# Kernel optimization log

Hardware: AMD Instinct MI355X
Metric: run time of the kernel (lower is better)

Reference implementation:

```python
import jax, jax.numpy as jnp
import numpy as np

B, N, IN_F, OUT_F, H = 16, 1024, 256, 256, 4
D = OUT_F // H  # head_dim = 64
NEG_SLOPE = 0.2


def setup_inputs() -> dict:
    key = jax.random.key(0)
    k1, k2, k3 = jax.random.split(key, 3)
    h = jax.random.normal(k1, (B, N, IN_F), dtype=jnp.float32)
    mask = jnp.ones((B, N), dtype=jnp.int32)
    W = jax.random.normal(k2, (OUT_F, IN_F), dtype=jnp.float32) * (1.0 / np.sqrt(IN_F))
    a = jax.random.normal(k3, (2 * D, 1), dtype=jnp.float32) * 0.1
    return {"h": h, "mask": mask, "W": W, "a": a}


def reference(h, mask, W, a):
    # Wh = h @ W.T -> (B, N, OUT_F) -> (B, H, N, D)
    Wh = jnp.einsum('bnf,of->bno', h, W)
    Wh = Wh.reshape(h.shape[0], h.shape[1], H, D).transpose(0, 2, 1, 3)
    # Additive split: cat([Wh_i, Wh_j]) @ a == Wh_i @ a1 + Wh_j @ a2 (same math,
    # avoids the O(N^2 * 2D) concat tensor)
    a1 = a[:D, 0]  # (D,)
    a2 = a[D:, 0]  # (D,)
    s1 = jnp.einsum('bhnd,d->bhn', Wh, a1)  # score for node i
    s2 = jnp.einsum('bhnd,d->bhn', Wh, a2)  # score for node j
    e = s1[:, :, :, None] + s2[:, :, None, :]          # (B, H, N, N)
    e = jnp.where(e >= 0, e, NEG_SLOPE * e)            # LeakyReLU(0.2)
    node_mask = mask.astype(bool)                      # (B, N)
    mm = node_mask[:, None, :, None] & node_mask[:, None, None, :]  # (B,1,N,N)
    e = jnp.where(mm, e, -jnp.inf)
    attn = jax.nn.softmax(e, axis=-1)
    # dropout is identity in eval mode
    attn = jnp.where(mm, attn, 0.0)
    h_prime = jnp.einsum('bhij,bhjd->bhid', attn, Wh)  # (B, H, N, D)
    h_prime = h_prime.transpose(0, 2, 1, 3).reshape(h.shape[0], h.shape[1], OUT_F)
    return h_prime * mask.astype(h_prime.dtype)[:, :, None]
```

## Files before the change

kernel.cpp:

```cpp
#include <hip/hip_runtime.h>

typedef short short8 __attribute__((ext_vector_type(8)));
typedef float floatx4 __attribute__((ext_vector_type(4)));
typedef float floatx16 __attribute__((ext_vector_type(16)));
typedef unsigned int u32;

#define NEG_SLOPE 0.2f

__device__ __forceinline__ u32 pk_rtne(float a, float b) {
    u32 ua = __float_as_uint(a); ua += 0x7fffu + ((ua >> 16) & 1u);
    u32 ub = __float_as_uint(b); ub += 0x7fffu + ((ub >> 16) & 1u);
    return __builtin_amdgcn_perm(ub, ua, 0x07060302);
}
__device__ __forceinline__ u32 pk_trunc(float a, float b) {
    return __builtin_amdgcn_perm(__float_as_uint(b), __float_as_uint(a), 0x07060302);
}
__device__ __forceinline__ void gl_lds16(const void* g, void* l) {
    __builtin_amdgcn_global_load_lds((__attribute__((address_space(1))) u32*)(void*)g,
                                     (__attribute__((address_space(3))) u32*)l, 16, 0, 0);
}

__global__ __launch_bounds__(256, 4) void k_wh(
    const float* __restrict__ hin, const int* __restrict__ mask,
    const float* __restrict__ W, const float* __restrict__ a,
    unsigned short* __restrict__ WhF, float2* __restrict__ E1F1,
    float2* __restrict__ E2F2)
{
    __shared__ unsigned short sBF[8 * 4 * 64 * 8];
    __shared__ float sV1[256], sV2[256];

    const int t = threadIdx.x;
    const int bi = blockIdx.x;
    const int mtile = bi & 255, hh = bi >> 8;
    const int m0g = mtile * 64;
    const int b = m0g >> 10, i0 = m0g & 1023;
    const int b4h = b * 4 + hh;
    const int wid = t >> 6, lane = t & 63;
    const int l15 = lane & 15, q = lane >> 4;

    sV1[t] = 0.f;
    sV2[t] = 0.f;
    __syncthreads();

    float vp1[8] = {0, 0, 0, 0, 0, 0, 0, 0};
    float vp2[8] = {0, 0, 0, 0, 0, 0, 0, 0};
    {
        const int c = t & 31;
        const int rb = t >> 5;
#pragma unroll
        for (int i = 0; i < 8; ++i) {
            int row = i * 8 + rb;
            const float* gp = &W[((size_t)(hh * 64 + row)) * 256 + c * 8];
            float4 w0 = *(const float4*)gp;
            float4 w1 = *(const float4*)(gp + 4);
            float a1r = a[row], a2r = a[64 + row];
            vp1[0] += a1r * w0.x; vp1[1] += a1r * w0.y; vp1[2] += a1r * w0.z; vp1[3] += a1r * w0.w;
            vp1[4] += a1r * w1.x; vp1[5] += a1r * w1.y; vp1[6] += a1r * w1.z; vp1[7] += a1r * w1.w;
            vp2[0] += a2r * w0.x; vp2[1] += a2r * w0.y; vp2[2] += a2r * w0.z; vp2[3] += a2r * w0.w;
            vp2[4] += a2r * w1.x; vp2[5] += a2r * w1.y; vp2[6] += a2r * w1.z; vp2[7] += a2r * w1.w;
            uint4 pv;
            pv.x = pk_rtne(w0.x, w0.y); pv.y = pk_rtne(w0.z, w0.w);
            pv.z = pk_rtne(w1.x, w1.y); pv.w = pk_rtne(w1.z, w1.w);
            int kt = c >> 2, qq = c & 3, nt = row >> 4, r15 = row & 15;
            int idx16 = (kt * 4 + nt) * 64 + qq * 16 + r15;
            *(uint4*)&sBF[(idx16 ^ kt) * 8] = pv;
        }
    }
#pragma unroll
    for (int j = 0; j < 8; ++j) {
        vp1[j] += __shfl_xor(vp1[j], 32, 64);
        vp2[j] += __shfl_xor(vp2[j], 32, 64);
    }
    if (lane < 32) {
        const int c = t & 31;
#pragma unroll
        for (int j = 0; j < 8; ++j) {
            atomicAdd(&sV1[c * 8 + j], vp1[j]);
            atomicAdd(&sV2[c * 8 + j], vp2[j]);
        }
    }
    __syncthreads();

    floatx4 acc[4];
#pragma unroll
    for (int nt = 0; nt < 4; ++nt) {
        floatx4 z = {0.f, 0.f, 0.f, 0.f};
        acc[nt] = z;
    }
    float s1a = 0.f, s2a = 0.f;
    const float* hrow = &hin[((size_t)(m0g + wid * 16 + l15)) * 256 + q * 8];
#pragma unroll
    for (int kt = 0; kt < 8; ++kt) {
        float4 h0 = *(const float4*)(hrow + kt * 32);
        float4 h1 = *(const float4*)(hrow + kt * 32 + 4);
        float4 v1a = *(const float4*)&sV1[kt * 32 + q * 8];
        float4 v1b = *(const float4*)&sV1[kt * 32 + q * 8 + 4];
        float4 v2a = *(const float4*)&sV2[kt * 32 + q * 8];
        float4 v2b = *(const float4*)&sV2[kt * 32 + q * 8 + 4];
        s1a += h0.x * v1a.x + h0.y * v1a.y + h0.z * v1a.z + h0.w * v1a.w
             + h1.x * v1b.x + h1.y * v1b.y + h1.z * v1b.z + h1.w * v1b.w;
        s2a += h0.x * v2a.x + h0.y * v2a.y + h0.z * v2a.z + h0.w * v2a.w
             + h1.x * v2b.x + h1.y * v2b.y + h1.z * v2b.z + h1.w * v2b.w;
        union { short8 s; uint4 u; } af;
        af.u.x = pk_rtne(h0.x, h0.y); af.u.y = pk_rtne(h0.z, h0.w);
        af.u.z = pk_rtne(h1.x, h1.y); af.u.w = pk_rtne(h1.z, h1.w);
#pragma unroll
        for (int nt = 0; nt < 4; ++nt) {
            int idx16 = (kt * 4 + nt) * 64 + lane;
            short8 bf = *(const short8*)&sBF[(idx16 ^ kt) * 8];
            acc[nt] = __builtin_amdgcn_mfma_f32_16x16x32_bf16(af.s, bf, acc[nt], 0, 0, 0);
        }
    }

    const int jt16 = (i0 >> 4) + wid;
    const int g = q & 1, jb = (q >> 1) * 4;
#pragma unroll
    for (int nt = 0; nt < 4; ++nt) {
        int nt32 = nt >> 1;
        int l31 = (nt & 1) * 16 + l15;
        uint2 pv;
        pv.x = pk_rtne(acc[nt][0], acc[nt][1]);
        pv.y = pk_rtne(acc[nt][2], acc[nt][3]);
        size_t idx = ((((size_t)b4h * 64 + jt16) * 2 + nt32) * 64 + (g * 32 + l31)) * 8 + jb;
        *(uint2*)&WhF[idx] = pv;
    }

    s1a += __shfl_xor(s1a, 16, 64); s1a += __shfl_xor(s1a, 32, 64);
    s2a += __shfl_xor(s2a, 16, 64); s2a += __shfl_xor(s2a, 32, 64);
    if (lane < 16) {
        int i = i0 + wid * 16 + lane;
        E1F1[(size_t)b4h * 1024 + i] = make_float2(__expf(s1a), __expf(NEG_SLOPE * s1a));
        int mj = mask[b * 1024 + i];
        E2F2[(size_t)b4h * 1024 + i] =
            make_float2(mj ? __expf(s2a) : 0.f, mj ? __expf(NEG_SLOPE * s2a) : 0.f);
    }
}

__global__ __launch_bounds__(256, 2) void k_attn(
    const int* __restrict__ mask,
    const unsigned short* __restrict__ WhF,
    const float2* __restrict__ E1F1, const float2* __restrict__ E2F2,
    float* __restrict__ out)
{
    __shared__ float2 sEF[1024];

    const int t = threadIdx.x;
    const int bi = blockIdx.x;
    const int b4h = bi & 63, ib = bi >> 6;
    const int b = b4h >> 2, hh = b4h & 3;
    const int i0 = ib * 128;
    const int wid = t >> 6, lane = t & 63;
    const int l31 = lane & 31, g = lane >> 5;
    const int iw = i0 + wid * 32;

    {
        const char* src = (const char*)(E2F2 + (size_t)b4h * 1024);
        gl_lds16(src + t * 16, (char*)sEF + t * 16);
        gl_lds16(src + 4096 + t * 16, (char*)sEF + 4096 + t * 16);
    }

    float2 e1 = E1F1[(size_t)b4h * 1024 + iw + l31];
    const float E1 = e1.x, F1 = e1.y;

    floatx16 acc0, acc1, accL;
#pragma unroll
    for (int r = 0; r < 16; ++r) { acc0[r] = 0.f; acc1[r] = 0.f; accL[r] = 0.f; }
    const short ob = (short)0x3F80;
    const short8 ones = {ob, ob, ob, ob, ob, ob, ob, ob};

    const char* gbase = (const char*)WhF + (size_t)b4h * 131072 + (size_t)lane * 16;

    __syncthreads();

    short8 nb0 = *(const short8*)(gbase);
    short8 nb1 = *(const short8*)(gbase + 1024);
    float4 nA0, nA1, nB0, nB1;
    {
        const float4* pA = (const float4*)&sEF[g * 4];
        const float4* pB = (const float4*)&sEF[8 + g * 4];
        nA0 = pA[0]; nA1 = pA[1]; nB0 = pB[0]; nB1 = pB[1];
    }

#pragma unroll 8
    for (int c = 0; c < 64; ++c) {
        const short8 bf0 = nb0, bf1 = nb1;
        const float4 eA0 = nA0, eA1 = nA1, eB0 = nB0, eB1 = nB1;
        {
            const int cn = (c + 1) & 63;
            nb0 = *(const short8*)(gbase + (size_t)cn * 2048);
            nb1 = *(const short8*)(gbase + (size_t)cn * 2048 + 1024);
            const float4* pA = (const float4*)&sEF[cn * 16 + g * 4];
            const float4* pB = (const float4*)&sEF[cn * 16 + 8 + g * 4];
            nA0 = pA[0]; nA1 = pA[1]; nB0 = pB[0]; nB1 = pB[1];
        }
        float w0 = fmaxf(E1 * eA0.x, F1 * eA0.y);
        float w1 = fmaxf(E1 * eA0.z, F1 * eA0.w);
        float w2 = fmaxf(E1 * eA1.x, F1 * eA1.y);
        float w3 = fmaxf(E1 * eA1.z, F1 * eA1.w);
        float w4 = fmaxf(E1 * eB0.x, F1 * eB0.y);
        float w5 = fmaxf(E1 * eB0.z, F1 * eB0.w);
        float w6 = fmaxf(E1 * eB1.x, F1 * eB1.y);
        float w7 = fmaxf(E1 * eB1.z, F1 * eB1.w);
        union { short8 s; u32 u[4]; } af;
        af.u[0] = pk_trunc(w0, w1);
        af.u[1] = pk_trunc(w2, w3);
        af.u[2] = pk_trunc(w4, w5);
        af.u[3] = pk_trunc(w6, w7);
        acc0 = __builtin_amdgcn_mfma_f32_32x32x16_bf16(af.s, bf0, acc0, 0, 0, 0);
        acc1 = __builtin_amdgcn_mfma_f32_32x32x16_bf16(af.s, bf1, acc1, 0, 0, 0);
        accL = __builtin_amdgcn_mfma_f32_32x32x16_bf16(af.s, ones, accL, 0, 0, 0);
    }

#pragma unroll
    for (int r = 0; r < 16; ++r) {
        int row = (r & 3) + 8 * (r >> 2) + 4 * g;
        int i = iw + row;
        float l = accL[r];
        int mi = mask[b * 1024 + i];
        float inv = (mi && l > 0.f) ? 1.0f / l : 0.f;
        size_t o = ((size_t)(b * 1024 + i)) * 256 + hh * 64;
        out[o + l31] = acc0[r] * inv;
        out[o + 32 + l31] = acc1[r] * inv;
    }
}

extern "C" void kernel_launch(void* const* d_in, const int* in_sizes, int n_in,
                              void* d_out, int out_size, void* d_ws, size_t ws_size,
                              hipStream_t stream) {
    const float* h = (const float*)d_in[0];
    const int* mask = (const int*)d_in[1];
    const float* W = (const float*)d_in[2];
    const float* a = (const float*)d_in[3];
    float* out = (float*)d_out;

    unsigned short* WhF = (unsigned short*)d_ws;
    float2* E1F1 = (float2*)((char*)d_ws + (size_t)64 * 64 * 2 * 64 * 8 * 2);
    float2* E2F2 = E1F1 + 64 * 1024;

    hipLaunchKernelGGL(k_wh, dim3(1024), dim3(256), 0, stream, h, mask, W, a, WhF, E1F1, E2F2);
    hipLaunchKernelGGL(k_attn, dim3(512), dim3(256), 0, stream, mask, WhF, E1F1, E2F2, out);
}
```

Before: 111.6 us.

## Split attention key range across warps with LDS reduction, double the grid

k_attn now covers 64 query rows per block instead of 128. Two warp pairs each process half of the 1024 keys, and their partial accumulators are combined through shared memory before normalisation. The grid doubles to 1024 blocks, launch bounds request 4 blocks per CU, and the WhF loads use a two-deep register prefetch. The aim is more parallelism and occupancy on the MFMA loop. The cost is about 25KB of extra LDS per block, a reduction step with a barrier, half the warps sitting idle in the epilogue, and duplicated WhF reads across blocks.

```diff
diff --git a/kernel.cpp b/kernel.cpp
--- a/kernel.cpp
+++ b/kernel.cpp
@@ -136,22 +136,24 @@
     }
 }
 
-__global__ __launch_bounds__(256, 2) void k_attn(
+__global__ __launch_bounds__(256, 4) void k_attn(
     const int* __restrict__ mask,
     const unsigned short* __restrict__ WhF,
     const float2* __restrict__ E1F1, const float2* __restrict__ E2F2,
     float* __restrict__ out)
 {
     __shared__ float2 sEF[1024];
+    __shared__ float sRed[2][64][49];
 
     const int t = threadIdx.x;
     const int bi = blockIdx.x;
     const int b4h = bi & 63, ib = bi >> 6;
     const int b = b4h >> 2, hh = b4h & 3;
-    const int i0 = ib * 128;
+    const int i0 = ib * 64;
     const int wid = t >> 6, lane = t & 63;
     const int l31 = lane & 31, g = lane >> 5;
-    const int iw = i0 + wid * 32;
+    const int rg = wid & 1, jh = wid >> 1;
+    const int iw = i0 + rg * 32;
 
     {
         const char* src = (const char*)(E2F2 + (size_t)b4h * 1024);
@@ -169,58 +171,105 @@
     const short8 ones = {ob, ob, ob, ob, ob, ob, ob, ob};
 
     const char* gbase = (const char*)WhF + (size_t)b4h * 131072 + (size_t)lane * 16;
-
-    __syncthreads();
-
-    short8 nb0 = *(const short8*)(gbase);
-    short8 nb1 = *(const short8*)(gbase + 1024);
+    const int cb = jh * 32;
+
+    short8 ga0 = *(const short8*)(gbase + (size_t)cb * 2048);
+    short8 ga1 = *(const short8*)(gbase + (size_t)cb * 2048 + 1024);
+    short8 gb0 = *(const short8*)(gbase + (size_t)(cb + 1) * 2048);
+    short8 gb1 = *(const short8*)(gbase + (size_t)(cb + 1) * 2048 + 1024);
+
+    __syncthreads();
+
     float4 nA0, nA1, nB0, nB1;
     {
-        const float4* pA = (const float4*)&sEF[g * 4];
-        const float4* pB = (const float4*)&sEF[8 + g * 4];
+        const float4* pA = (const float4*)&sEF[cb * 16 + g * 4];
+        const float4* pB = (const float4*)&sEF[cb * 16 + 8 + g * 4];
         nA0 = pA[0]; nA1 = pA[1]; nB0 = pB[0]; nB1 = pB[1];
     }
 
-#pragma unroll 8
-    for (int c = 0; c < 64; ++c) {
-        const short8 bf0 = nb0, bf1 = nb1;
-        const float4 eA0 = nA0, eA1 = nA1, eB0 = nB0, eB1 = nB1;
+#pragma unroll 4
+    for (int cr = 0; cr < 32; cr += 2) {
         {
-            const int cn = (c + 1) & 63;
-            nb0 = *(const short8*)(gbase + (size_t)cn * 2048);
-            nb1 = *(const short8*)(gbase + (size_t)cn * 2048 + 1024);
+            const float4 eA0 = nA0, eA1 = nA1, eB0 = nB0, eB1 = nB1;
+            const int cn = cb + ((cr + 1) & 31);
             const float4* pA = (const float4*)&sEF[cn * 16 + g * 4];
             const float4* pB = (const float4*)&sEF[cn * 16 + 8 + g * 4];
             nA0 = pA[0]; nA1 = pA[1]; nB0 = pB[0]; nB1 = pB[1];
-        }
-        float w0 = fmaxf(E1 * eA0.x, F1 * eA0.y);
-        float w1 = fmaxf(E1 * eA0.z, F1 * eA0.w);
-        float w2 = fmaxf(E1 * eA1.x, F1 * eA1.y);
-        float w3 = fmaxf(E1 * eA1.z, F1 * eA1.w);
-        float w4 = fmaxf(E1 * eB0.x, F1 * eB0.y);
-        float w5 = fmaxf(E1 * eB0.z, F1 * eB0.w);
-        float w6 = fmaxf(E1 * eB1.x, F1 * eB1.y);
-        float w7 = fmaxf(E1 * eB1.z, F1 * eB1.w);
-        union { short8 s; u32 u[4]; } af;
-        af.u[0] = pk_trunc(w0, w1);
-        af.u[1] = pk_trunc(w2, w3);
-        af.u[2] = pk_trunc(w4, w5);
-        af.u[3] = pk_trunc(w6, w7);
-        acc0 = __builtin_amdgcn_mfma_f32_32x32x16_bf16(af.s, bf0, acc0, 0, 0, 0);
-        acc1 = __builtin_amdgcn_mfma_f32_32x32x16_bf16(af.s, bf1, acc1, 0, 0, 0);
-        accL = __builtin_amdgcn_mfma_f32_32x32x16_bf16(af.s, ones, accL, 0, 0, 0);
-    }
-
-#pragma unroll
-    for (int r = 0; r < 16; ++r) {
-        int row = (r & 3) + 8 * (r >> 2) + 4 * g;
-        int i = iw + row;
-        float l = accL[r];
-        int mi = mask[b * 1024 + i];
-        float inv = (mi && l > 0.f) ? 1.0f / l : 0.f;
-        size_t o = ((size_t)(b * 1024 + i)) * 256 + hh * 64;
-        out[o + l31] = acc0[r] * inv;
-        out[o + 32 + l31] = acc1[r] * inv;
+            const short8 bf0 = ga0, bf1 = ga1;
+            const int cg = cb + ((cr + 2) & 31);
+            ga0 = *(const short8*)(gbase + (size_t)cg * 2048);
+            ga1 = *(const short8*)(gbase + (size_t)cg * 2048 + 1024);
+            float w0 = fmaxf(E1 * eA0.x, F1 * eA0.y);
+            float w1 = fmaxf(E1 * eA0.z, F1 * eA0.w);
+            float w2 = fmaxf(E1 * eA1.x, F1 * eA1.y);
+            float w3 = fmaxf(E1 * eA1.z, F1 * eA1.w);
+            float w4 = fmaxf(E1 * eB0.x, F1 * eB0.y);
+            float w5 = fmaxf(E1 * eB0.z, F1 * eB0.w);
+            float w6 = fmaxf(E1 * eB1.x, F1 * eB1.y);
+            float w7 = fmaxf(E1 * eB1.z, F1 * eB1.w);
+            union { short8 s; u32 u[4]; } af;
+            af.u[0] = pk_trunc(w0, w1);
+            af.u[1] = pk_trunc(w2, w3);
+            af.u[2] = pk_trunc(w4, w5);
+            af.u[3] = pk_trunc(w6, w7);
+            acc0 = __builtin_amdgcn_mfma_f32_32x32x16_bf16(af.s, bf0, acc0, 0, 0, 0);
+            acc1 = __builtin_amdgcn_mfma_f32_32x32x16_bf16(af.s, bf1, acc1, 0, 0, 0);
+            accL = __builtin_amdgcn_mfma_f32_32x32x16_bf16(af.s, ones, accL, 0, 0, 0);
+        }
+        {
+            const float4 eA0 = nA0, eA1 = nA1, eB0 = nB0, eB1 = nB1;
+            const int cn = cb + ((cr + 2) & 31);
+            const float4* pA = (const float4*)&sEF[cn * 16 + g * 4];
+            const float4* pB = (const float4*)&sEF[cn * 16 + 8 + g * 4];
+            nA0 = pA[0]; nA1 = pA[1]; nB0 = pB[0]; nB1 = pB[1];
+            const short8 bf0 = gb0, bf1 = gb1;
+            const int cg = cb + ((cr + 3) & 31);
+            gb0 = *(const short8*)(gbase + (size_t)cg * 2048);
+            gb1 = *(const short8*)(gbase + (size_t)cg * 2048 + 1024);
+            float w0 = fmaxf(E1 * eA0.x, F1 * eA0.y);
+            float w1 = fmaxf(E1 * eA0.z, F1 * eA0.w);
+            float w2 = fmaxf(E1 * eA1.x, F1 * eA1.y);
+            float w3 = fmaxf(E1 * eA1.z, F1 * eA1.w);
+            float w4 = fmaxf(E1 * eB0.x, F1 * eB0.y);
+            float w5 = fmaxf(E1 * eB0.z, F1 * eB0.w);
+            float w6 = fmaxf(E1 * eB1.x, F1 * eB1.y);
+            float w7 = fmaxf(E1 * eB1.z, F1 * eB1.w);
+            union { short8 s; u32 u[4]; } af;
+            af.u[0] = pk_trunc(w0, w1);
+            af.u[1] = pk_trunc(w2, w3);
+            af.u[2] = pk_trunc(w4, w5);
+            af.u[3] = pk_trunc(w6, w7);
+            acc0 = __builtin_amdgcn_mfma_f32_32x32x16_bf16(af.s, bf0, acc0, 0, 0, 0);
+            acc1 = __builtin_amdgcn_mfma_f32_32x32x16_bf16(af.s, bf1, acc1, 0, 0, 0);
+            accL = __builtin_amdgcn_mfma_f32_32x32x16_bf16(af.s, ones, accL, 0, 0, 0);
+        }
+    }
+
+    if (jh == 1) {
+        float* d = &sRed[rg][lane][0];
+#pragma unroll
+        for (int r = 0; r < 16; ++r) {
+            d[r] = acc0[r]; d[16 + r] = acc1[r]; d[32 + r] = accL[r];
+        }
+    }
+    __syncthreads();
+    if (jh == 0) {
+        const float* d = &sRed[rg][lane][0];
+#pragma unroll
+        for (int r = 0; r < 16; ++r) {
+            acc0[r] += d[r]; acc1[r] += d[16 + r]; accL[r] += d[32 + r];
+        }
+#pragma unroll
+        for (int r = 0; r < 16; ++r) {
+            int row = (r & 3) + 8 * (r >> 2) + 4 * g;
+            int i = iw + row;
+            float l = accL[r];
+            int mi = mask[b * 1024 + i];
+            float inv = (mi && l > 0.f) ? 1.0f / l : 0.f;
+            size_t o = ((size_t)(b * 1024 + i)) * 256 + hh * 64;
+            out[o + l31] = acc0[r] * inv;
+            out[o + 32 + l31] = acc1[r] * inv;
+        }
     }
 }
 
@@ -238,5 +287,5 @@
     float2* E2F2 = E1F1 + 64 * 1024;
 
     hipLaunchKernelGGL(k_wh, dim3(1024), dim3(256), 0, stream, h, mask, W, a, WhF, E1F1, E2F2);
-    hipLaunchKernelGGL(k_attn, dim3(512), dim3(256), 0, stream, mask, WhF, E1F1, E2F2, out);
-}
+    hipLaunchKernelGGL(k_attn, dim3(1024), dim3(256), 0, stream, mask, WhF, E1F1, E2F2, out);
+}
```

Measured after the change: 103.2 us. 1.08x faster.
